# Optimization experiments

Measured on AMD Instinct MI355X. Metric: run time of the kernel, lower is better.

## Reference

```python
import jax, jax.numpy as jnp
import numpy as np

NUM_HEADS = 16
WINDOW_SIZE = 256  # config.window_size; layer is 'local'


def setup_inputs() -> dict:
    key = jax.random.key(0)
    ks = jax.random.split(key, 8)
    B, S, H = 4, 2048, 1024
    scale = 1.0 / np.sqrt(H)
    return {
        "x": jax.random.normal(ks[0], (B, S, H), dtype=jnp.float32),
        "x_clean": jax.random.normal(ks[1], (B, S, H), dtype=jnp.float32),
        "ablation_mask": jax.random.uniform(ks[2], (B, S, H), dtype=jnp.float32),
        "Wq": jax.random.normal(ks[3], (H, H), dtype=jnp.float32) * scale,
        "Wk": jax.random.normal(ks[4], (H, H), dtype=jnp.float32) * scale,
        "Wv": jax.random.normal(ks[5], (H, H), dtype=jnp.float32) * scale,
        "Wo": jax.random.normal(ks[6], (H, H), dtype=jnp.float32) * scale,
        "bo": jnp.zeros((H,), dtype=jnp.float32),
    }


def reference(x, x_clean, ablation_mask, Wq, Wk, Wv, Wo, bo):
    B, S, H = x.shape
    nh, hd = NUM_HEADS, H // NUM_HEADS

    def proj(inp, W):  # torch Linear: inp @ W.T -> split heads -> [B, nh, S, hd]
        return jnp.einsum('bsh,oh->bso', inp, W).reshape(B, S, nh, hd).transpose(0, 2, 1, 3)

    q = proj(x, Wq)
    k = proj(x_clean, Wk)
    v = proj(x_clean, Wv)

    # NOTE: original applies NO 1/sqrt(head_dim) scaling.
    scores = jnp.einsum('bnsd,bntd->bnst', q, k)  # [B, nh, S, S]

    i = jnp.arange(S)[:, None]
    j = jnp.arange(S)[None, :]
    # local mask: forbid future (j > i) OR too-far past (j <= i - window)
    masked = (j > i) | (j <= i - WINDOW_SIZE)
    scores = jnp.where(masked[None, None, :, :], -jnp.inf, scores)

    attn = jax.nn.softmax(scores, axis=-1)
    context = jnp.einsum('bnst,bntd->bnsd', attn, v)          # [B, nh, S, hd]
    context = context.transpose(0, 2, 1, 3).reshape(B, S, H)   # merge heads
    context = context * ablation_mask
    return jnp.einsum('bsh,oh->bso', context, Wo) + bo
```

## Files before the change

kernel.cpp:

```cpp
#include <hip/hip_runtime.h>
#include <hip/hip_bf16.h>
#include <cstddef>

#define SB 4
#define SS 2048
#define SH 1024
#define NH 16
#define HD 64
#define WIN 256

typedef __attribute__((ext_vector_type(8))) short bf16x8;
typedef __attribute__((ext_vector_type(8))) _Float16 f16x8;
typedef __attribute__((ext_vector_type(2))) __fp16 fp16v2;
typedef __attribute__((ext_vector_type(4))) float f32x4;

static __device__ __forceinline__ ushort2 pk_bf16(float a, float b) {
    __hip_bfloat162 h = __float22bfloat162_rn(make_float2(a, b));
    union { __hip_bfloat162 h2; ushort2 u2; } u;
    u.h2 = h;
    return u.u2;
}
static __device__ __forceinline__ unsigned short pk1(float a) {
    return pk_bf16(a, 0.f).x;
}

static __device__ __forceinline__ void async16(const void* gptr, void* lptr) {
    __builtin_amdgcn_global_load_lds(
        (const __attribute__((address_space(1))) unsigned int*)gptr,
        (__attribute__((address_space(3))) unsigned int*)lptr, 16, 0, 0);
}

#define CFENCE() asm volatile("" ::: "memory")

__global__ __launch_bounds__(256) void cvt_all(
    const float* __restrict__ x,  const float* __restrict__ xc,
    const float* __restrict__ Wq, const float* __restrict__ Wk,
    const float* __restrict__ Wv, const float* __restrict__ Wo,
    _Float16* __restrict__ xh,  _Float16* __restrict__ xch,
    _Float16* __restrict__ Wqh, _Float16* __restrict__ Wkh,
    _Float16* __restrict__ Wvh, _Float16* __restrict__ Woh)
{
    const int I4 = SB * SS * SH / 4;
    const int W4 = SH * SH / 4;
    int idx = blockIdx.x * 256 + threadIdx.x;
    const float* src;
    _Float16* dst;
    int off;
    if (idx < I4) { src = x; dst = xh; off = idx; }
    else if (idx < 2 * I4) { src = xc; dst = xch; off = idx - I4; }
    else {
        int r = idx - 2 * I4;
        int wi = r >> 18;
        off = r & (W4 - 1);
        src = (wi == 0) ? Wq : (wi == 1) ? Wk : (wi == 2) ? Wv : Wo;
        dst = (wi == 0) ? Wqh : (wi == 1) ? Wkh : (wi == 2) ? Wvh : Woh;
    }
    float4 v = ((const float4*)src)[off];
    union { fp16v2 h[2]; uint2 u; } t;
    t.h[0] = __builtin_amdgcn_cvt_pkrtz(v.x, v.y);
    t.h[1] = __builtin_amdgcn_cvt_pkrtz(v.z, v.w);
    ((uint2*)dst)[off] = t.u;
}

static __device__ __forceinline__ void gemm8_core(
    const _Float16* __restrict__ A, const _Float16* __restrict__ W,
    int m0, int n0, unsigned short* __restrict__ smem, f32x4 (&acc)[4][4])
{
    const int K = SH;
    const int NT = K / 64;
    const int tid = threadIdx.x;
    const int w = tid >> 6, lane = tid & 63;
    const int wm = (w >> 2) * 64;
    const int wn = (w & 3) * 64;
    const int lrow = lane & 15;
    const int lk8 = (lane >> 4) * 8;
    const int swz = (lrow & 7) << 3;

    const int srow = w * 8 + (lane >> 3);
    const int scol = ((lane & 7) ^ ((lane >> 3) & 7)) << 3;
    const _Float16* aS = A + (size_t)(m0 + srow) * K + scol;
    const _Float16* bS = W + (size_t)(n0 + srow) * K + scol;

    auto stA = [&](int tile, int half) {
        async16(aS + (size_t)(half * 64) * K + tile * 64,
                smem + ((tile & 1) << 13) + half * 4096 + w * 512);
    };
    auto stB = [&](int tile, int half) {
        async16(bS + (size_t)(half * 128) * K + tile * 64,
                smem + 16384 + ((tile & 1) << 14) + half * 8192 + w * 512);
        async16(bS + (size_t)(half * 128 + 64) * K + tile * 64,
                smem + 16384 + ((tile & 1) << 14) + half * 8192 + 4096 + w * 512);
    };

    f16x8 a[2][2];
    f16x8 b[2][2][2];

    stA(0, 0); stA(0, 1);
    stB(0, 0); stB(0, 1);
    stB(1, 0); stB(1, 1);
    asm volatile("s_waitcnt vmcnt(4)" ::: "memory");
    __builtin_amdgcn_s_barrier();
    CFENCE();

    for (int t = 0; t < NT; ++t) {
        const int cur = t & 1;
        unsigned short* LA = smem + (cur << 13);
        unsigned short* LB = smem + 16384 + (cur << 14);

#pragma unroll
        for (int m = 0; m < 2; ++m)
#pragma unroll
            for (int ks = 0; ks < 2; ++ks)
                a[m][ks] = *(const f16x8*)(LA + (wm + m * 16 + lrow) * 64 + ((ks * 32 + lk8) ^ swz));
#pragma unroll
        for (int n = 0; n < 2; ++n)
#pragma unroll
            for (int ks = 0; ks < 2; ++ks)
                b[0][n][ks] = *(const f16x8*)(LB + (wn + n * 16 + lrow) * 64 + ((ks * 32 + lk8) ^ swz));
        if (t + 1 < NT) stA(t + 1, 0);
        CFENCE();
        __builtin_amdgcn_s_barrier();
        CFENCE();
        asm volatile("s_waitcnt lgkmcnt(0)" ::: "memory");
        __builtin_amdgcn_s_setprio(1);
#pragma unroll
        for (int ks = 0; ks < 2; ++ks)
#pragma unroll
            for (int m = 0; m < 2; ++m)
#pragma unroll
                for (int n = 0; n < 2; ++n)
                    acc[m][n] = __builtin_amdgcn_mfma_f32_16x16x32_f16(a[m][ks], b[0][n][ks], acc[m][n], 0, 0, 0);
        __builtin_amdgcn_s_setprio(0);
        CFENCE();
        __builtin_amdgcn_s_barrier();
        CFENCE();

#pragma unroll
        for (int n = 0; n < 2; ++n)
#pragma unroll
            for (int ks = 0; ks < 2; ++ks)
                b[1][n][ks] = *(const f16x8*)(LB + (wn + 32 + n * 16 + lrow) * 64 + ((ks * 32 + lk8) ^ swz));
        if (t + 1 < NT) stA(t + 1, 1);
        CFENCE();
        __builtin_amdgcn_s_barrier();
        CFENCE();
        asm volatile("s_waitcnt lgkmcnt(0)" ::: "memory");
        __builtin_amdgcn_s_setprio(1);
#pragma unroll
        for (int ks = 0; ks < 2; ++ks)
#pragma unroll
            for (int m = 0; m < 2; ++m)
#pragma unroll
                for (int n = 0; n < 2; ++n)
                    acc[m][2 + n] = __builtin_amdgcn_mfma_f32_16x16x32_f16(a[m][ks], b[1][n][ks], acc[m][2 + n], 0, 0, 0);
        __builtin_amdgcn_s_setprio(0);
        CFENCE();
        __builtin_amdgcn_s_barrier();
        CFENCE();

#pragma unroll
        for (int m = 0; m < 2; ++m)
#pragma unroll
            for (int ks = 0; ks < 2; ++ks)
                a[m][ks] = *(const f16x8*)(LA + (wm + 32 + m * 16 + lrow) * 64 + ((ks * 32 + lk8) ^ swz));
        if (t + 2 < NT) stB(t + 2, 0);
        CFENCE();
        __builtin_amdgcn_s_barrier();
        CFENCE();
        asm volatile("s_waitcnt lgkmcnt(0)" ::: "memory");
        __builtin_amdgcn_s_setprio(1);
#pragma unroll
        for (int ks = 0; ks < 2; ++ks)
#pragma unroll
            for (int m = 0; m < 2; ++m)
#pragma unroll
                for (int n = 0; n < 2; ++n)
                    acc[2 + m][2 + n] = __builtin_amdgcn_mfma_f32_16x16x32_f16(a[m][ks], b[1][n][ks], acc[2 + m][2 + n], 0, 0, 0);
        __builtin_amdgcn_s_setprio(0);
        CFENCE();
        __builtin_amdgcn_s_barrier();
        CFENCE();

        if (t + 2 < NT) stB(t + 2, 1);
        CFENCE();
        __builtin_amdgcn_s_barrier();
        CFENCE();
        __builtin_amdgcn_s_setprio(1);
#pragma unroll
        for (int ks = 0; ks < 2; ++ks)
#pragma unroll
            for (int m = 0; m < 2; ++m)
#pragma unroll
                for (int n = 0; n < 2; ++n)
                    acc[2 + m][n] = __builtin_amdgcn_mfma_f32_16x16x32_f16(a[m][ks], b[0][n][ks], acc[2 + m][n], 0, 0, 0);
        __builtin_amdgcn_s_setprio(0);
        if (t < NT - 2) asm volatile("s_waitcnt vmcnt(4)" ::: "memory");
        else            asm volatile("s_waitcnt vmcnt(0)" ::: "memory");
        __builtin_amdgcn_s_barrier();
        CFENCE();
    }
    CFENCE();
}

__global__ __launch_bounds__(512, 2) void gemm_qkv8(
    const _Float16* __restrict__ xh, const _Float16* __restrict__ xch,
    const _Float16* __restrict__ Wqh, const _Float16* __restrict__ Wkh,
    const _Float16* __restrict__ Wvh,
    _Float16* __restrict__ Qh, _Float16* __restrict__ Kh,
    unsigned short* __restrict__ Vt)
{
    __shared__ __align__(16) unsigned short smem[49152];
    const int z = blockIdx.z;
    const _Float16* A = (z == 0) ? xh : xch;
    const _Float16* W = (z == 0) ? Wqh : (z == 1) ? Wkh : Wvh;
    const int m0 = blockIdx.x * 128;
    const int n0 = blockIdx.y * 256;

    f32x4 acc[4][4];
#pragma unroll
    for (int i = 0; i < 4; ++i)
#pragma unroll
        for (int j = 0; j < 4; ++j)
            acc[i][j] = (f32x4){0.f, 0.f, 0.f, 0.f};

    gemm8_core(A, W, m0, n0, smem, acc);

    const int tid = threadIdx.x;
    const int w = tid >> 6, lane = tid & 63;
    const int wm = (w >> 2) * 64, wn = (w & 3) * 64;
    const int lrow = lane & 15;
    const int rq = (lane >> 4) * 4;
    const int M = SB * SS, N = SH;

    if (z < 2) {
        _Float16* C = (z == 0) ? Qh : Kh;
        _Float16* T = (_Float16*)smem;
#pragma unroll
        for (int m = 0; m < 4; ++m)
#pragma unroll
            for (int n = 0; n < 4; ++n)
#pragma unroll
                for (int r = 0; r < 4; ++r)
                    T[(wm + m * 16 + rq + r) * 264 + wn + n * 16 + lrow] = (_Float16)acc[m][n][r];
        __syncthreads();
#pragma unroll
        for (int u = 0; u < 8; ++u) {
            int slot = u * 512 + tid;
            int row = slot >> 5;
            int c8 = (slot & 31) * 8;
            *(uint4*)(C + (size_t)(m0 + row) * N + n0 + c8) =
                *(const uint4*)&T[row * 264 + c8];
        }
    } else {
        unsigned short* T = smem;
#pragma unroll
        for (int n = 0; n < 4; ++n)
#pragma unroll
            for (int m = 0; m < 4; ++m) {
                int rt = wn + n * 16 + lrow;
                *(ushort4*)&T[rt * 136 + wm + m * 16 + rq] = make_ushort4(
                    pk1(acc[m][n][0]), pk1(acc[m][n][1]),
                    pk1(acc[m][n][2]), pk1(acc[m][n][3]));
            }
        __syncthreads();
#pragma unroll
        for (int u = 0; u < 8; ++u) {
            int slot = u * 512 + tid;
            int row = slot >> 4;
            int m8 = (slot & 15) * 8;
            *(uint4*)(Vt + (size_t)(n0 + row) * M + m0 + m8) =
                *(const uint4*)&T[row * 136 + m8];
        }
    }
}

__global__ __launch_bounds__(512, 2) void gemm_o8(
    const _Float16* __restrict__ A, const _Float16* __restrict__ W,
    const float* __restrict__ bias, float* __restrict__ C)
{
    __shared__ __align__(16) unsigned short smem[49152];
    const int m0 = blockIdx.x * 128;
    const int n0 = blockIdx.y * 256;

    f32x4 acc[4][4];
#pragma unroll
    for (int i = 0; i < 4; ++i)
#pragma unroll
        for (int j = 0; j < 4; ++j)
            acc[i][j] = (f32x4){0.f, 0.f, 0.f, 0.f};

    gemm8_core(A, W, m0, n0, smem, acc);

    const int tid = threadIdx.x;
    const int w = tid >> 6, lane = tid & 63;
    const int wm = (w >> 2) * 64, wn = (w & 3) * 64;
    const int lrow = lane & 15;
    const int rq = (lane >> 4) * 4;
    const int N = SH;

#pragma unroll
    for (int m = 0; m < 4; ++m) {
        int rbase = m0 + wm + m * 16 + rq;
#pragma unroll
        for (int n = 0; n < 4; ++n) {
            int col = n0 + wn + n * 16 + lrow;
            float badd = bias[col];
#pragma unroll
            for (int r = 0; r < 4; ++r)
                C[(size_t)(rbase + r) * N + col] = acc[m][n][r] + badd;
        }
    }
}

__global__ __launch_bounds__(512, 4) void attn5(
    const _Float16* Qg, const _Float16* __restrict__ Kg,
    const unsigned short* __restrict__ Vtg, const float* __restrict__ amask,
    _Float16* ctxg)
{
    __shared__ __align__(16) _Float16 K_s[2][2 * 64 * 32];
    __shared__ __align__(16) unsigned short V_s[2][2 * 64 * 32];
    __shared__ __align__(16) unsigned short P_s[8][32 * 72];

    const int t = threadIdx.x;
    const int wave = t >> 6, lane = t & 63;
    const int id = blockIdx.x;
    const int qb = id >> 6;
    const int pr = id & 63;
    const int h = pr & 15, b = pr >> 4;
    const int t0 = qb * 256;
    const int wq = t0 + wave * 32;
    const int lrow = lane & 15;
    const int lk8 = (lane >> 4) * 8;
    const int rq = (lane >> 4) * 4;
    const int M = SB * SS;
    unsigned short* P = P_s[wave];

    const int ski = t >> 8;
    const int srow = (t & 255) >> 2;
    const int se8 = (t & 3) * 8;

    f16x8 qf[2][2];
#pragma unroll
    for (int i = 0; i < 2; ++i)
#pragma unroll
        for (int ki = 0; ki < 2; ++ki)
            qf[i][ki] = *(const f16x8*)(Qg +
                (size_t)(b * SS + wq + i * 16 + lrow) * SH + h * HD + ki * 32 + lk8);

    f32x4 o[2][4];
    float lsum[2][4];
#pragma unroll
    for (int i = 0; i < 2; ++i)
#pragma unroll
        for (int j = 0; j < 4; ++j) o[i][j] = (f32x4){0.f, 0.f, 0.f, 0.f};
#pragma unroll
    for (int i = 0; i < 2; ++i)
#pragma unroll
        for (int r = 0; r < 4; ++r) lsum[i][r] = 0.f;

    int cl0 = t0 - (WIN - 1);
    cl0 = cl0 < 0 ? 0 : cl0;
    const int c_lo = cl0 >> 6;
    const int c_hi = (t0 >> 6) + 3;

    auto stage = [&](int c, int buf) {
        const int key0 = c * 64;
        async16(Kg + (size_t)(b * SS + key0 + srow) * SH + h * HD + ski * 32 + se8,
                (_Float16*)K_s[buf] + wave * 512);
        async16(Vtg + (size_t)(h * HD + srow) * M + b * SS + key0 + ski * 32 + se8,
                (unsigned short*)V_s[buf] + wave * 512);
    };

    stage(c_lo, c_lo & 1);
    __syncthreads();

    for (int c = c_lo; c <= c_hi; ++c) {
        const int cur = c & 1;
        if (c < c_hi) stage(c + 1, cur ^ 1);
        const int key0 = c * 64;
        if (key0 <= wq + 31 && key0 + 63 >= wq - (WIN - 1)) {
            const _Float16* Kc = (const _Float16*)K_s[cur];
            const unsigned short* Vc = (const unsigned short*)V_s[cur];

            f32x4 s[2][4];
#pragma unroll
            for (int i = 0; i < 2; ++i)
#pragma unroll
                for (int j = 0; j < 4; ++j) s[i][j] = (f32x4){0.f, 0.f, 0.f, 0.f};
#pragma unroll
            for (int ki = 0; ki < 2; ++ki)
#pragma unroll
                for (int j = 0; j < 4; ++j) {
                    f16x8 bh = *(const f16x8*)&Kc[ki * 2048 + (j * 16 + lrow) * 32 + lk8];
#pragma unroll
                    for (int i = 0; i < 2; ++i)
                        s[i][j] = __builtin_amdgcn_mfma_f32_16x16x32_f16(qf[i][ki], bh, s[i][j], 0, 0, 0);
                }

#pragma unroll
            for (int i = 0; i < 2; ++i)
#pragma unroll
                for (int j = 0; j < 4; ++j) {
                    int jg = key0 + j * 16 + lrow;
#pragma unroll
                    for (int r = 0; r < 4; ++r) {
                        int qg = wq + i * 16 + rq + r;
                        float p = (jg <= qg && jg > qg - WIN) ? __expf(s[i][j][r]) : 0.f;
                        lsum[i][r] += p;
                        P[(i * 16 + rq + r) * 72 + j * 16 + lrow] = pk1(p);
                    }
                }

#pragma unroll
            for (int ki = 0; ki < 2; ++ki) {
                bf16x8 pf[2];
#pragma unroll
                for (int i = 0; i < 2; ++i)
                    pf[i] = *(const bf16x8*)&P[(i * 16 + lrow) * 72 + ki * 32 + lk8];
#pragma unroll
                for (int j = 0; j < 4; ++j) {
                    bf16x8 vf = *(const bf16x8*)&Vc[ki * 2048 + (j * 16 + lrow) * 32 + lk8];
#pragma unroll
                    for (int i = 0; i < 2; ++i)
                        o[i][j] = __builtin_amdgcn_mfma_f32_16x16x32_bf16(pf[i], vf, o[i][j], 0, 0, 0);
                }
            }
        }
        __syncthreads();
    }

#pragma unroll
    for (int i = 0; i < 2; ++i)
#pragma unroll
        for (int r = 0; r < 4; ++r) {
#pragma unroll
            for (int m = 1; m < 16; m <<= 1)
                lsum[i][r] += __shfl_xor(lsum[i][r], m);
        }

    _Float16* Pf = (_Float16*)P;
#pragma unroll
    for (int i = 0; i < 2; ++i)
#pragma unroll
        for (int r = 0; r < 4; ++r) {
            float inv = 1.f / lsum[i][r];
#pragma unroll
            for (int j = 0; j < 4; ++j)
                Pf[(i * 16 + rq + r) * 72 + j * 16 + lrow] = (_Float16)(o[i][j][r] * inv);
        }
#pragma unroll
    for (int u = 0; u < 4; ++u) {
        int slot = u * 64 + lane;
        int ro = slot >> 3;
        int d8 = (slot & 7) * 8;
        f16x8 v = *(const f16x8*)&Pf[ro * 72 + d8];
        size_t g = (size_t)(b * SS + wq + ro) * SH + h * HD + d8;
        float4 ma = *(const float4*)(amask + g);
        float4 mb = *(const float4*)(amask + g + 4);
        f16x8 rs;
        rs[0] = (_Float16)((float)v[0] * ma.x);
        rs[1] = (_Float16)((float)v[1] * ma.y);
        rs[2] = (_Float16)((float)v[2] * ma.z);
        rs[3] = (_Float16)((float)v[3] * ma.w);
        rs[4] = (_Float16)((float)v[4] * mb.x);
        rs[5] = (_Float16)((float)v[5] * mb.y);
        rs[6] = (_Float16)((float)v[6] * mb.z);
        rs[7] = (_Float16)((float)v[7] * mb.w);
        *(f16x8*)(ctxg + g) = rs;
    }
}

extern "C" void kernel_launch(void* const* d_in, const int* in_sizes, int n_in,
                              void* d_out, int out_size, void* d_ws, size_t ws_size,
                              hipStream_t stream)
{
    const float* x     = (const float*)d_in[0];
    const float* xc    = (const float*)d_in[1];
    const float* amask = (const float*)d_in[2];
    const float* Wq    = (const float*)d_in[3];
    const float* Wk    = (const float*)d_in[4];
    const float* Wv    = (const float*)d_in[5];
    const float* Wo    = (const float*)d_in[6];
    const float* bo    = (const float*)d_in[7];
    float* out = (float*)d_out;

    const int M = SB * SS;
    const size_t BUF = (size_t)M * SH;
    const size_t WBUF = (size_t)SH * SH;
    _Float16* xh  = (_Float16*)d_ws;
    _Float16* xch = xh + BUF;
    _Float16* Qh  = xch + BUF;
    _Float16* Kh  = Qh + BUF;
    unsigned short* Vt = (unsigned short*)(Kh + BUF);
    _Float16* Wqh = (_Float16*)(Vt + BUF);
    _Float16* Wkh = Wqh + WBUF;
    _Float16* Wvh = Wkh + WBUF;
    _Float16* Woh = Wvh + WBUF;
    _Float16* ctx = Qh;

    const int total4 = 2 * (M * SH / 4) + 4 * (SH * SH / 4);
    hipLaunchKernelGGL(cvt_all, dim3(total4 / 256), dim3(256), 0, stream,
                       x, xc, Wq, Wk, Wv, Wo, xh, xch, Wqh, Wkh, Wvh, Woh);

    hipLaunchKernelGGL(gemm_qkv8, dim3(M / 128, SH / 256, 3), dim3(512), 0, stream,
                       xh, xch, Wqh, Wkh, Wvh, Qh, Kh, Vt);

    hipLaunchKernelGGL(attn5, dim3((SS / 256) * NH * SB), dim3(512), 0, stream,
                       Qh, Kh, Vt, amask, ctx);

    hipLaunchKernelGGL(gemm_o8, dim3(M / 128, SH / 256), dim3(512), 0, stream,
                       ctx, Woh, bo, out);
}
```

Before: 271.9 us.

## Restructure GEMM main loop into two phases with full A fragment reuse

The 8-wave GEMM inner loop goes from four MFMA phases to two. Each wave now loads all four A row fragments once per K-tile and reuses them against two B halves. The global-to-LDS prefetch schedule and vmcnt waits are reordered to match, and fewer barriers and LDS reads are issued per tile. The cost is more live A registers per wave, and the new ordering of async copies and waits risks LDS hazards if the counts are off.

```diff
diff --git a/kernel.cpp b/kernel.cpp
--- a/kernel.cpp
+++ b/kernel.cpp
@@ -92,13 +92,13 @@
                 smem + 16384 + ((tile & 1) << 14) + half * 8192 + 4096 + w * 512);
     };
 
-    f16x8 a[2][2];
-    f16x8 b[2][2][2];
+    f16x8 a[4][2];
+    f16x8 b[2][2];
 
     stA(0, 0); stA(0, 1);
     stB(0, 0); stB(0, 1);
-    stB(1, 0); stB(1, 1);
-    asm volatile("s_waitcnt vmcnt(4)" ::: "memory");
+    stB(1, 0);
+    asm volatile("s_waitcnt vmcnt(2)" ::: "memory");
     __builtin_amdgcn_s_barrier();
     CFENCE();
 
@@ -108,7 +108,7 @@
         unsigned short* LB = smem + 16384 + (cur << 14);
 
 #pragma unroll
-        for (int m = 0; m < 2; ++m)
+        for (int m = 0; m < 4; ++m)
 #pragma unroll
             for (int ks = 0; ks < 2; ++ks)
                 a[m][ks] = *(const f16x8*)(LA + (wm + m * 16 + lrow) * 64 + ((ks * 32 + lk8) ^ swz));
@@ -116,9 +116,11 @@
         for (int n = 0; n < 2; ++n)
 #pragma unroll
             for (int ks = 0; ks < 2; ++ks)
-                b[0][n][ks] = *(const f16x8*)(LB + (wn + n * 16 + lrow) * 64 + ((ks * 32 + lk8) ^ swz));
-        if (t + 1 < NT) stA(t + 1, 0);
-        CFENCE();
+                b[n][ks] = *(const f16x8*)(LB + (wn + n * 16 + lrow) * 64 + ((ks * 32 + lk8) ^ swz));
+        if (t + 1 < NT) { stA(t + 1, 0); stA(t + 1, 1); stB(t + 1, 1); }
+        CFENCE();
+        if (t + 1 < NT) asm volatile("s_waitcnt vmcnt(6)" ::: "memory");
+        else            asm volatile("s_waitcnt vmcnt(0)" ::: "memory");
         __builtin_amdgcn_s_barrier();
         CFENCE();
         asm volatile("s_waitcnt lgkmcnt(0)" ::: "memory");
@@ -126,10 +128,10 @@
 #pragma unroll
         for (int ks = 0; ks < 2; ++ks)
 #pragma unroll
-            for (int m = 0; m < 2; ++m)
+            for (int m = 0; m < 4; ++m)
 #pragma unroll
                 for (int n = 0; n < 2; ++n)
-                    acc[m][n] = __builtin_amdgcn_mfma_f32_16x16x32_f16(a[m][ks], b[0][n][ks], acc[m][n], 0, 0, 0);
+                    acc[m][n] = __builtin_amdgcn_mfma_f32_16x16x32_f16(a[m][ks], b[n][ks], acc[m][n], 0, 0, 0);
         __builtin_amdgcn_s_setprio(0);
         CFENCE();
         __builtin_amdgcn_s_barrier();
@@ -139,8 +141,8 @@
         for (int n = 0; n < 2; ++n)
 #pragma unroll
             for (int ks = 0; ks < 2; ++ks)
-                b[1][n][ks] = *(const f16x8*)(LB + (wn + 32 + n * 16 + lrow) * 64 + ((ks * 32 + lk8) ^ swz));
-        if (t + 1 < NT) stA(t + 1, 1);
+                b[n][ks] = *(const f16x8*)(LB + (wn + 32 + n * 16 + lrow) * 64 + ((ks * 32 + lk8) ^ swz));
+        if (t + 2 < NT) stB(t + 2, 0);
         CFENCE();
         __builtin_amdgcn_s_barrier();
         CFENCE();
@@ -149,53 +151,14 @@
 #pragma unroll
         for (int ks = 0; ks < 2; ++ks)
 #pragma unroll
-            for (int m = 0; m < 2; ++m)
+            for (int m = 0; m < 4; ++m)
 #pragma unroll
                 for (int n = 0; n < 2; ++n)
-                    acc[m][2 + n] = __builtin_amdgcn_mfma_f32_16x16x32_f16(a[m][ks], b[1][n][ks], acc[m][2 + n], 0, 0, 0);
+                    acc[m][2 + n] = __builtin_amdgcn_mfma_f32_16x16x32_f16(a[m][ks], b[n][ks], acc[m][2 + n], 0, 0, 0);
         __builtin_amdgcn_s_setprio(0);
-        CFENCE();
-        __builtin_amdgcn_s_barrier();
-        CFENCE();
-
-#pragma unroll
-        for (int m = 0; m < 2; ++m)
-#pragma unroll
-            for (int ks = 0; ks < 2; ++ks)
-                a[m][ks] = *(const f16x8*)(LA + (wm + 32 + m * 16 + lrow) * 64 + ((ks * 32 + lk8) ^ swz));
-        if (t + 2 < NT) stB(t + 2, 0);
-        CFENCE();
-        __builtin_amdgcn_s_barrier();
-        CFENCE();
-        asm volatile("s_waitcnt lgkmcnt(0)" ::: "memory");
-        __builtin_amdgcn_s_setprio(1);
-#pragma unroll
-        for (int ks = 0; ks < 2; ++ks)
-#pragma unroll
-            for (int m = 0; m < 2; ++m)
-#pragma unroll
-                for (int n = 0; n < 2; ++n)
-                    acc[2 + m][2 + n] = __builtin_amdgcn_mfma_f32_16x16x32_f16(a[m][ks], b[1][n][ks], acc[2 + m][2 + n], 0, 0, 0);
-        __builtin_amdgcn_s_setprio(0);
-        CFENCE();
-        __builtin_amdgcn_s_barrier();
-        CFENCE();
-
-        if (t + 2 < NT) stB(t + 2, 1);
-        CFENCE();
-        __builtin_amdgcn_s_barrier();
-        CFENCE();
-        __builtin_amdgcn_s_setprio(1);
-#pragma unroll
-        for (int ks = 0; ks < 2; ++ks)
-#pragma unroll
-            for (int m = 0; m < 2; ++m)
-#pragma unroll
-                for (int n = 0; n < 2; ++n)
-                    acc[2 + m][n] = __builtin_amdgcn_mfma_f32_16x16x32_f16(a[m][ks], b[0][n][ks], acc[2 + m][n], 0, 0, 0);
-        __builtin_amdgcn_s_setprio(0);
-        if (t < NT - 2) asm volatile("s_waitcnt vmcnt(4)" ::: "memory");
-        else            asm volatile("s_waitcnt vmcnt(0)" ::: "memory");
+        if (t < NT - 2)       asm volatile("s_waitcnt vmcnt(4)" ::: "memory");
+        else if (t == NT - 2) asm volatile("s_waitcnt vmcnt(2)" ::: "memory");
+        else                  asm volatile("s_waitcnt vmcnt(0)" ::: "memory");
         __builtin_amdgcn_s_barrier();
         CFENCE();
     }
```

Measured after the change: 265.8 us. -2.2%, faster.
